# Performance work log

Hardware: AMD Instinct MI355X
Metric: run time of the kernel (lower is better)

Reference implementation:

```python
import jax, jax.numpy as jnp
import numpy as np

H = 100  # hidden size


def _lstm_final_hidden(x, W_ih, W_hh, b_ih, b_hh):
    # x: [B, T, 4] -> final hidden state h_T: [B, H]
    B, T, _ = x.shape
    # Precompute input contribution for all time steps: [B, T, 4H]
    xW = jnp.einsum('btf,gf->btg', x, W_ih) + b_ih + b_hh
    xW = jnp.transpose(xW, (1, 0, 2))  # [T, B, 4H] for scan over time

    def step(carry, xt):
        h, c = carry
        gates = xt + h @ W_hh.T  # [B, 4H]
        i, f, g, o = jnp.split(gates, 4, axis=-1)  # torch gate order: i, f, g, o
        c = jax.nn.sigmoid(f) * c + jax.nn.sigmoid(i) * jnp.tanh(g)
        h = jax.nn.sigmoid(o) * jnp.tanh(c)
        return (h, c), None

    h0 = jnp.zeros((B, H), dtype=x.dtype)
    (hT, _), _ = jax.lax.scan(step, (h0, h0), xW)
    return hT


def setup_inputs() -> dict:
    key = jax.random.key(0)
    k1, k2, k3, k4, k5 = jax.random.split(key, 5)
    n_cells, T = 4096, 128
    short_ttf = jax.random.normal(k1, (n_cells, 3, T, 4), dtype=jnp.float32)
    W_ih = jax.random.normal(k2, (4 * H, 4), dtype=jnp.float32) * 0.1
    # torch init: uniform(-0.05, 0.05) for weight_hh
    W_hh = jax.random.uniform(k3, (4 * H, H), dtype=jnp.float32, minval=-0.05, maxval=0.05)
    b_ih = jax.random.normal(k4, (4 * H,), dtype=jnp.float32) * 0.1
    b_hh = jax.random.normal(k5, (4 * H,), dtype=jnp.float32) * 0.1
    return {"short_ttf": short_ttf, "W_ih": W_ih, "W_hh": W_hh, "b_ih": b_ih, "b_hh": b_hh}


def reference(short_ttf, W_ih, W_hh, b_ih, b_hh):
    # short_ttf: [n_cells, 3, T, 4]. Each of the 3 sub-sequences per cell is run
    # through the same LSTM; last-step hidden states are concatenated -> [n_cells, 3H].
    n_cells, three, T, F = short_ttf.shape
    x = short_ttf.reshape(n_cells * three, T, F)  # batch all sequences together
    hT = _lstm_final_hidden(x, W_ih, W_hh, b_ih, b_hh)  # [n_cells*3, H]
    return hT.reshape(n_cells, three * H)  # [n_cells, 300]
```

## Files before the change

kernel.cpp:

```cpp
#include <hip/hip_runtime.h>
#include <cstdint>


#define H_UNITS 100
#define T_STEPS 128
#define S_BLK   16
#define NSEQ    12288
#define NBLK    (NSEQ / S_BLK)
#define NTILE   25
#define KSTR    136
#define LOG2E   1.4426950408889634f
#define TWO_L   2.8853900817779268f

typedef __attribute__((ext_vector_type(8))) _Float16 halfx8;
typedef __attribute__((ext_vector_type(8))) unsigned short ushortx8;
typedef __attribute__((ext_vector_type(4))) float floatx4;
typedef __attribute__((ext_vector_type(2))) float floatx2;

__device__ __forceinline__ unsigned short f32_to_f16u(float x) {
    _Float16 h = (_Float16)x;
    return __builtin_bit_cast(unsigned short, h);
}
__device__ __forceinline__ float f16u_to_f32(unsigned short u) {
    _Float16 h = __builtin_bit_cast(_Float16, u);
    return (float)h;
}
#if __has_builtin(__builtin_amdgcn_exp2f)
__device__ __forceinline__ float fexp2(float x) { return __builtin_amdgcn_exp2f(x); }
#else
__device__ __forceinline__ float fexp2(float x) { return exp2f(x); }
#endif

__global__ void lstm_prep_pack(const float* __restrict__ W_ih,
                               const float* __restrict__ W_hh,
                               const float* __restrict__ b_ih,
                               const float* __restrict__ b_hh,
                               ushortx8* __restrict__ Bpack) {
    int t = blockIdx.x * 256 + threadIdx.x;
    if (t >= NTILE * 4 * 64) return;
    int lane = t & 63;
    int kc   = (t >> 6) & 3;
    int tile = t >> 8;
    int m    = lane & 15;
    int n;
    if (tile < 24) {
        int pr = tile >> 1, half = tile & 1;
        int reg = m & 3,   qr   = m >> 2;
        int g = (reg >> 1) + 2 * half;
        int u = 8 * pr + 2 * qr + (reg & 1);
        n = g * 100 + u;
    } else {
        n = (m & 3) * 100 + 96 + (m >> 2);
    }
    float sc = (n >= 200 && n < 300) ? (2.0f * LOG2E) : LOG2E;
    int k0 = kc * 32 + ((lane >> 4) & 3) * 8;
    ushortx8 v;
#pragma unroll
    for (int j = 0; j < 8; ++j) {
        int k = k0 + j;
        unsigned short w = 0;
        if (k < 100) {
            w = f32_to_f16u(W_hh[n * 100 + k] * sc);
        } else if (k < 108) {
            w = f32_to_f16u(W_ih[n * 4 + ((k - 100) & 3)] * sc);
        } else if (k < 112) {
            float wf = W_ih[n * 4 + (k - 108)] * sc;
            unsigned short hi = f32_to_f16u(wf);
            w = f32_to_f16u(wf - f16u_to_f32(hi));
        } else if (k == 112) {
            float bb = (b_ih[n] + b_hh[n]) * sc;
            w = f32_to_f16u(bb);
        } else if (k == 113) {
            float bb = (b_ih[n] + b_hh[n]) * sc;
            unsigned short hi = f32_to_f16u(bb);
            w = f32_to_f16u(bb - f16u_to_f32(hi));
        }
        v[j] = w;
    }
    Bpack[t] = v;
}

__global__ void __launch_bounds__(256, 4)
lstm_main(const float* __restrict__ x, const ushortx8* __restrict__ Bpack,
          float* __restrict__ out) {
    __shared__ __align__(16) unsigned short s_A[2][16 * KSTR];
    __shared__ __align__(16) ushortx8       s_W[NTILE * 64];
    __shared__ __align__(16) ushortx8       s_W24[3 * 64];

    const int tid  = threadIdx.x;
    const int lane = tid & 63;
    const int wavu = __builtin_amdgcn_readfirstlane(tid >> 6);
    const int seq0 = blockIdx.x * S_BLK;
    const int m    = lane & 15;
    const int quad = lane >> 4;
    const int q2   = quad << 1;

    halfx8 wfrag[6][3];
#pragma unroll
    for (int s = 0; s < 6; ++s) {
        int tile = 2 * (wavu + (s >> 1) * 4) + (s & 1);
#pragma unroll
        for (int kc = 0; kc < 3; ++kc)
            wfrag[s][kc] = __builtin_bit_cast(halfx8, Bpack[(tile * 4 + kc + 1) * 64 + lane]);
    }
    for (int i = tid; i < NTILE * 64; i += 256)
        s_W[i] = Bpack[(i >> 6) * 256 + (i & 63)];
    if (tid < 3 * 64)
        s_W24[tid] = Bpack[(24 * 4 + 1 + (tid >> 6)) * 64 + (tid & 63)];

    const int rt = tid - 128;
    const int rs = rt & 15, rc = (rt >> 4) & 7;
    const float* xb = x + (size_t)(seq0 + rs) * (T_STEPS * 4) + (rc & 3);

    for (int i = tid; i < (2 * 16 * KSTR) / 2; i += 256)
        ((unsigned int*)s_A)[i] = 0u;
    float x0 = 0.0f;
    if (tid >= 128) x0 = xb[0];
    __syncthreads();
    if (tid >= 128) {
        unsigned short hi = f32_to_f16u(x0);
        if (rc < 4) {
            s_A[0][rs * KSTR + 100 + rc] = hi;
            s_A[0][rs * KSTR + 108 + rc] = hi;
        } else {
            s_A[0][rs * KSTR + 104 + (rc - 4)] =
                f32_to_f16u(x0 - f16u_to_f32(hi));
        }
    } else if (tid < 32) {
        s_A[tid >> 4][(tid & 15) * KSTR + 112] = 0x3C00;
    } else if (tid < 64) {
        int d = tid - 32;
        s_A[d >> 4][(d & 15) * KSTR + 113] = 0x3C00;
    }
    __syncthreads();

    floatx2 cpr[3];
#pragma unroll
    for (int it = 0; it < 3; ++it) cpr[it] = (floatx2){0.0f, 0.0f};
    float c24 = 0.0f;

    const int rowOff = m * KSTR;
    const int aOff   = rowOff + quad * 8;

    for (int t = 0; t < T_STEPS; ++t) {
        const int bR = t & 1;
        const unsigned short* base  = s_A[bR];
        unsigned short*       baseW = s_A[bR ^ 1];

        float xnext = 0.0f;
        if (tid >= 128) {
            int tn = t + 1; if (tn > T_STEPS - 1) tn = T_STEPS - 1;
            xnext = xb[tn * 4];
        }

        halfx8 hh[4];
#pragma unroll
        for (int kc = 0; kc < 4; ++kc)
            hh[kc] = *(const halfx8*)(base + aOff + kc * 32);

        const bool last = (t == T_STEPS - 1);

        auto gemm4 = [&](halfx8 w0, halfx8 w1, halfx8 w2, halfx8 w3) {
            floatx4 a = {0.0f, 0.0f, 0.0f, 0.0f};
            a = __builtin_amdgcn_mfma_f32_16x16x32_f16(w0, hh[0], a, 0, 0, 0);
            a = __builtin_amdgcn_mfma_f32_16x16x32_f16(w1, hh[1], a, 0, 0, 0);
            a = __builtin_amdgcn_mfma_f32_16x16x32_f16(w2, hh[2], a, 0, 0, 0);
            a = __builtin_amdgcn_mfma_f32_16x16x32_f16(w3, hh[3], a, 0, 0, 0);
            return a;
        };

        auto activatePair = [&](floatx4 aA, floatx4 aB, floatx2& cm, int p) {
            floatx2 ei = {fexp2(aA[0]), fexp2(aA[1])};
            floatx2 ef = {fexp2(aA[2]), fexp2(aA[3])};
            floatx2 eg = {fexp2(aB[0]), fexp2(aB[1])};
            floatx2 eo = {fexp2(aB[2]), fexp2(aB[3])};
            floatx2 a  = ei + 1.0f;
            floatx2 b  = ef + 1.0f;
            floatx2 d  = eg + 1.0f;
            floatx2 p1 = eo + 1.0f;
            floatx2 e2s = eg * TWO_L - TWO_L;
            floatx2 q  = a * d;
            floatx2 qb = q * b;
            floatx2 r  = {__builtin_amdgcn_rcpf(qb[0]), __builtin_amdgcn_rcpf(qb[1])};
            floatx2 eib = ei * b;
            floatx2 efq = ef * q;
            floatx2 tt  = eib * e2s;
            floatx2 nm  = efq * cm + tt;
            floatx2 c2  = nm * r;
            cm = c2;
            floatx2 cc = {fminf(c2[0], 115.0f), fminf(c2[1], 115.0f)};
            floatx2 ec = {fexp2(cc[0]), fexp2(cc[1])};
            floatx2 p2 = ec + 1.0f;
            floatx2 nu = ec - 1.0f;
            floatx2 pp = p1 * p2;
            floatx2 r2 = {__builtin_amdgcn_rcpf(pp[0]), __builtin_amdgcn_rcpf(pp[1])};
            floatx2 eon = eo * nu;
            floatx2 hv  = eon * r2;
            if (!last) {
                unsigned int pk = (unsigned int)f32_to_f16u(hv[0]) |
                                  ((unsigned int)f32_to_f16u(hv[1]) << 16);
                *(unsigned int*)&baseW[rowOff + 8 * p + q2] = pk;
            } else {
                *(floatx2*)&out[(size_t)(seq0 + m) * H_UNITS + 8 * p + q2] = hv;
            }
        };

#pragma unroll
        for (int it = 0; it < 3; ++it) {
            int p = wavu + it * 4;
            halfx8 w0A = __builtin_bit_cast(halfx8, s_W[(2 * p) * 64 + lane]);
            halfx8 w0B = __builtin_bit_cast(halfx8, s_W[(2 * p + 1) * 64 + lane]);
            floatx4 aA = gemm4(w0A, wfrag[2 * it][0], wfrag[2 * it][1], wfrag[2 * it][2]);
            floatx4 aB = gemm4(w0B, wfrag[2 * it + 1][0], wfrag[2 * it + 1][1], wfrag[2 * it + 1][2]);
            activatePair(aA, aB, cpr[it], p);
        }

        if (wavu == 0) {
            halfx8 w0 = __builtin_bit_cast(halfx8, s_W[24 * 64 + lane]);
            halfx8 w1 = __builtin_bit_cast(halfx8, s_W24[0 * 64 + lane]);
            halfx8 w2 = __builtin_bit_cast(halfx8, s_W24[1 * 64 + lane]);
            halfx8 w3 = __builtin_bit_cast(halfx8, s_W24[2 * 64 + lane]);
            floatx4 acc = gemm4(w0, w1, w2, w3);
            float ei = fexp2(acc[0]);
            float ef = fexp2(acc[1]);
            float eg = fexp2(acc[2]);
            float eo = fexp2(acc[3]);
            float a  = 1.0f + ei, b = 1.0f + ef;
            float d  = eg + 1.0f;
            float e2s = fmaf(eg, TWO_L, -TWO_L);
            float q  = a * d;
            float r  = __builtin_amdgcn_rcpf(q * b);
            float nm = fmaf(ef * q, c24, (ei * b) * e2s);
            float c2 = nm * r;
            c24 = c2;
            float cc = fminf(c2, 115.0f);
            float ec = fexp2(cc);
            float r2 = __builtin_amdgcn_rcpf((1.0f + eo) * (ec + 1.0f));
            float h  = (eo * (ec - 1.0f)) * r2;
            if (!last) {
                baseW[rowOff + 96 + quad] = f32_to_f16u(h);
            } else {
                out[(size_t)(seq0 + m) * H_UNITS + 96 + quad] = h;
            }
        }

        if (tid >= 128 && !last) {
            unsigned short hi = f32_to_f16u(xnext);
            if (rc < 4) {
                baseW[rs * KSTR + 100 + rc] = hi;
                baseW[rs * KSTR + 108 + rc] = hi;
            } else {
                baseW[rs * KSTR + 104 + (rc - 4)] =
                    f32_to_f16u(xnext - f16u_to_f32(hi));
            }
        }
        __syncthreads();
    }
}

extern "C" void kernel_launch(void* const* d_in, const int* in_sizes, int n_in,
                              void* d_out, int out_size, void* d_ws, size_t ws_size,
                              hipStream_t stream) {
    const float* x    = (const float*)d_in[0];
    const float* W_ih = (const float*)d_in[1];
    const float* W_hh = (const float*)d_in[2];
    const float* b_ih = (const float*)d_in[3];
    const float* b_hh = (const float*)d_in[4];
    ushortx8* Bpack = (ushortx8*)d_ws;

    lstm_prep_pack<<<25, 256, 0, stream>>>(W_ih, W_hh, b_ih, b_hh, Bpack);
    lstm_main<<<NBLK, 256, 0, stream>>>(x, Bpack, (float*)d_out);
}
```

Measured before the change: 289.2 us.

## Split LSTM gate tiles across eight waves per block instead of four

Doubles the block to 512 threads so each of eight waves handles fewer gate tiles per time step. Waves 0-7 keep their first tile pair's weights fully in registers, waves 0-3 take a second pair from shared memory, and wave 4 takes the leftover tile. The aim is a shorter serial critical path per recurrence step through more wave-level parallelism. In exchange it needs more waves per CU and sync across 8 waves, and load is uneven across waves.

```diff
diff --git a/kernel.cpp b/kernel.cpp
--- a/kernel.cpp
+++ b/kernel.cpp
@@ -80,12 +80,11 @@
     Bpack[t] = v;
 }
 
-__global__ void __launch_bounds__(256, 4)
+__global__ void __launch_bounds__(512, 4)
 lstm_main(const float* __restrict__ x, const ushortx8* __restrict__ Bpack,
           float* __restrict__ out) {
     __shared__ __align__(16) unsigned short s_A[2][16 * KSTR];
-    __shared__ __align__(16) ushortx8       s_W[NTILE * 64];
-    __shared__ __align__(16) ushortx8       s_W24[3 * 64];
+    __shared__ __align__(16) ushortx8       s_W[36 * 64];
 
     const int tid  = threadIdx.x;
     const int lane = tid & 63;
@@ -95,29 +94,32 @@
     const int quad = lane >> 4;
     const int q2   = quad << 1;
 
-    halfx8 wfrag[6][3];
+    halfx8 wfA[4], wfB[4];
 #pragma unroll
-    for (int s = 0; s < 6; ++s) {
-        int tile = 2 * (wavu + (s >> 1) * 4) + (s & 1);
-#pragma unroll
-        for (int kc = 0; kc < 3; ++kc)
-            wfrag[s][kc] = __builtin_bit_cast(halfx8, Bpack[(tile * 4 + kc + 1) * 64 + lane]);
-    }
-    for (int i = tid; i < NTILE * 64; i += 256)
-        s_W[i] = Bpack[(i >> 6) * 256 + (i & 63)];
-    if (tid < 3 * 64)
-        s_W24[tid] = Bpack[(24 * 4 + 1 + (tid >> 6)) * 64 + (tid & 63)];
-
-    const int rt = tid - 128;
-    const int rs = rt & 15, rc = (rt >> 4) & 7;
+    for (int kc = 0; kc < 4; ++kc) {
+        wfA[kc] = __builtin_bit_cast(halfx8, Bpack[((2 * wavu) * 4 + kc) * 64 + lane]);
+        wfB[kc] = __builtin_bit_cast(halfx8, Bpack[((2 * wavu + 1) * 4 + kc) * 64 + lane]);
+    }
+
+    for (int i = tid; i < 36 * 64; i += 512) {
+        int f = i >> 6, ln = i & 63;
+        int tile = (f < 32) ? (16 + (f >> 2)) : 24;
+        int kc   = (f < 32) ? (f & 3) : (f - 32);
+        s_W[i] = Bpack[(tile * 4 + kc) * 64 + ln];
+    }
+
+    const int rt   = tid - 320;
+    const bool refr = (rt >= 0) && (rt < 128);
+    const int rtc  = refr ? rt : 0;
+    const int rs   = rtc & 15, rc = (rtc >> 4) & 7;
     const float* xb = x + (size_t)(seq0 + rs) * (T_STEPS * 4) + (rc & 3);
 
-    for (int i = tid; i < (2 * 16 * KSTR) / 2; i += 256)
+    for (int i = tid; i < (2 * 16 * KSTR) / 2; i += 512)
         ((unsigned int*)s_A)[i] = 0u;
     float x0 = 0.0f;
-    if (tid >= 128) x0 = xb[0];
+    if (refr) x0 = xb[0];
     __syncthreads();
-    if (tid >= 128) {
+    if (refr) {
         unsigned short hi = f32_to_f16u(x0);
         if (rc < 4) {
             s_A[0][rs * KSTR + 100 + rc] = hi;
@@ -126,21 +128,19 @@
             s_A[0][rs * KSTR + 104 + (rc - 4)] =
                 f32_to_f16u(x0 - f16u_to_f32(hi));
         }
-    } else if (tid < 32) {
-        s_A[tid >> 4][(tid & 15) * KSTR + 112] = 0x3C00;
     } else if (tid < 64) {
-        int d = tid - 32;
-        s_A[d >> 4][(d & 15) * KSTR + 113] = 0x3C00;
+        int b = tid >> 5, r = (tid >> 1) & 15, col = 112 + (tid & 1);
+        s_A[b][r * KSTR + col] = 0x3C00;
     }
     __syncthreads();
 
-    floatx2 cpr[3];
-#pragma unroll
-    for (int it = 0; it < 3; ++it) cpr[it] = (floatx2){0.0f, 0.0f};
-    float c24 = 0.0f;
+    floatx2 c0 = {0.0f, 0.0f};
+    floatx2 c1 = {0.0f, 0.0f};
+    float   c24 = 0.0f;
 
     const int rowOff = m * KSTR;
     const int aOff   = rowOff + quad * 8;
+    const int hb     = wavu * 512 + lane;
 
     for (int t = 0; t < T_STEPS; ++t) {
         const int bR = t & 1;
@@ -148,7 +148,7 @@
         unsigned short*       baseW = s_A[bR ^ 1];
 
         float xnext = 0.0f;
-        if (tid >= 128) {
+        if (refr) {
             int tn = t + 1; if (tn > T_STEPS - 1) tn = T_STEPS - 1;
             xnext = xb[tn * 4];
         }
@@ -205,21 +205,29 @@
             }
         };
 
-#pragma unroll
-        for (int it = 0; it < 3; ++it) {
-            int p = wavu + it * 4;
-            halfx8 w0A = __builtin_bit_cast(halfx8, s_W[(2 * p) * 64 + lane]);
-            halfx8 w0B = __builtin_bit_cast(halfx8, s_W[(2 * p + 1) * 64 + lane]);
-            floatx4 aA = gemm4(w0A, wfrag[2 * it][0], wfrag[2 * it][1], wfrag[2 * it][2]);
-            floatx4 aB = gemm4(w0B, wfrag[2 * it + 1][0], wfrag[2 * it + 1][1], wfrag[2 * it + 1][2]);
-            activatePair(aA, aB, cpr[it], p);
-        }
-
-        if (wavu == 0) {
-            halfx8 w0 = __builtin_bit_cast(halfx8, s_W[24 * 64 + lane]);
-            halfx8 w1 = __builtin_bit_cast(halfx8, s_W24[0 * 64 + lane]);
-            halfx8 w2 = __builtin_bit_cast(halfx8, s_W24[1 * 64 + lane]);
-            halfx8 w3 = __builtin_bit_cast(halfx8, s_W24[2 * 64 + lane]);
+        {
+            floatx4 aA = gemm4(wfA[0], wfA[1], wfA[2], wfA[3]);
+            floatx4 aB = gemm4(wfB[0], wfB[1], wfB[2], wfB[3]);
+            activatePair(aA, aB, c0, wavu);
+        }
+
+        if (wavu < 4) {
+            halfx8 wa0 = __builtin_bit_cast(halfx8, s_W[hb + 0 * 64]);
+            halfx8 wa1 = __builtin_bit_cast(halfx8, s_W[hb + 1 * 64]);
+            halfx8 wa2 = __builtin_bit_cast(halfx8, s_W[hb + 2 * 64]);
+            halfx8 wa3 = __builtin_bit_cast(halfx8, s_W[hb + 3 * 64]);
+            floatx4 aA = gemm4(wa0, wa1, wa2, wa3);
+            halfx8 wb0 = __builtin_bit_cast(halfx8, s_W[hb + 256 + 0 * 64]);
+            halfx8 wb1 = __builtin_bit_cast(halfx8, s_W[hb + 256 + 1 * 64]);
+            halfx8 wb2 = __builtin_bit_cast(halfx8, s_W[hb + 256 + 2 * 64]);
+            halfx8 wb3 = __builtin_bit_cast(halfx8, s_W[hb + 256 + 3 * 64]);
+            floatx4 aB = gemm4(wb0, wb1, wb2, wb3);
+            activatePair(aA, aB, c1, 8 + wavu);
+        } else if (wavu == 4) {
+            halfx8 w0 = __builtin_bit_cast(halfx8, s_W[2048 + 0 * 64 + lane]);
+            halfx8 w1 = __builtin_bit_cast(halfx8, s_W[2048 + 1 * 64 + lane]);
+            halfx8 w2 = __builtin_bit_cast(halfx8, s_W[2048 + 2 * 64 + lane]);
+            halfx8 w3 = __builtin_bit_cast(halfx8, s_W[2048 + 3 * 64 + lane]);
             floatx4 acc = gemm4(w0, w1, w2, w3);
             float ei = fexp2(acc[0]);
             float ef = fexp2(acc[1]);
@@ -244,7 +252,7 @@
             }
         }
 
-        if (tid >= 128 && !last) {
+        if (refr && !last) {
             unsigned short hi = f32_to_f16u(xnext);
             if (rc < 4) {
                 baseW[rs * KSTR + 100 + rc] = hi;
@@ -269,5 +277,5 @@
     ushortx8* Bpack = (ushortx8*)d_ws;
 
     lstm_prep_pack<<<25, 256, 0, stream>>>(W_ih, W_hh, b_ih, b_hh, Bpack);
-    lstm_main<<<NBLK, 256, 0, stream>>>(x, Bpack, (float*)d_out);
-}
+    lstm_main<<<NBLK, 512, 0, stream>>>(x, Bpack, (float*)d_out);
+}
```

Measured after the change: 283.2 us (median of 2 runs). 2.1% less time.

## Run each 16-sequence LSTM block on a single wavefront with register-resident weights

Applied to the files above, without the earlier changes.

Replaces the 4-wave block with a single 64-thread wavefront that computes all 25 gate tiles for its 16 sequences. 20 tiles of W_hh are held in registers and the rest are read from shared memory. Using one wave removes the per-step __syncthreads and the double-buffered hidden-state array, so h is updated in place. The cost is much higher register pressure, possible spills, and fewer waves to hide MFMA and transcendental latency, since each wave now does four times the serial work per step.

```diff
diff --git a/kernel.cpp b/kernel.cpp
--- a/kernel.cpp
+++ b/kernel.cpp
@@ -80,83 +80,68 @@
     Bpack[t] = v;
 }
 
-__global__ void __launch_bounds__(256, 4)
+__global__ void __launch_bounds__(64, 1)
 lstm_main(const float* __restrict__ x, const ushortx8* __restrict__ Bpack,
           float* __restrict__ out) {
-    __shared__ __align__(16) unsigned short s_A[2][16 * KSTR];
-    __shared__ __align__(16) ushortx8       s_W[NTILE * 64];
-    __shared__ __align__(16) ushortx8       s_W24[3 * 64];
-
-    const int tid  = threadIdx.x;
-    const int lane = tid & 63;
-    const int wavu = __builtin_amdgcn_readfirstlane(tid >> 6);
-    const int seq0 = blockIdx.x * S_BLK;
+    __shared__ __align__(16) unsigned short s_h[16 * KSTR];
+    __shared__ __align__(16) ushortx8       s_W[20 * 64];
+
+    const int lane = threadIdx.x & 63;
     const int m    = lane & 15;
     const int quad = lane >> 4;
     const int q2   = quad << 1;
-
-    halfx8 wfrag[6][3];
-#pragma unroll
-    for (int s = 0; s < 6; ++s) {
-        int tile = 2 * (wavu + (s >> 1) * 4) + (s & 1);
-#pragma unroll
-        for (int kc = 0; kc < 3; ++kc)
-            wfrag[s][kc] = __builtin_bit_cast(halfx8, Bpack[(tile * 4 + kc + 1) * 64 + lane]);
-    }
-    for (int i = tid; i < NTILE * 64; i += 256)
-        s_W[i] = Bpack[(i >> 6) * 256 + (i & 63)];
-    if (tid < 3 * 64)
-        s_W24[tid] = Bpack[(24 * 4 + 1 + (tid >> 6)) * 64 + (tid & 63)];
-
-    const int rt = tid - 128;
-    const int rs = rt & 15, rc = (rt >> 4) & 7;
-    const float* xb = x + (size_t)(seq0 + rs) * (T_STEPS * 4) + (rc & 3);
-
-    for (int i = tid; i < (2 * 16 * KSTR) / 2; i += 256)
-        ((unsigned int*)s_A)[i] = 0u;
-    float x0 = 0.0f;
-    if (tid >= 128) x0 = xb[0];
-    __syncthreads();
-    if (tid >= 128) {
+    const int seq0 = blockIdx.x * S_BLK;
+
+    halfx8 wfA[10][4], wfB[10][4];
+#pragma unroll
+    for (int p = 0; p < 10; ++p)
+#pragma unroll
+        for (int kc = 0; kc < 4; ++kc) {
+            wfA[p][kc] = __builtin_bit_cast(halfx8, Bpack[((2 * p) * 4 + kc) * 64 + lane]);
+            wfB[p][kc] = __builtin_bit_cast(halfx8, Bpack[((2 * p + 1) * 4 + kc) * 64 + lane]);
+        }
+    for (int i = lane; i < 20 * 64; i += 64) {
+        int f = i >> 6, ln = i & 63;
+        int tile = (f < 16) ? (20 + (f >> 2)) : 24;
+        int kc   = (f < 16) ? (f & 3) : (f - 16);
+        s_W[i] = Bpack[(tile * 4 + kc) * 64 + ln];
+    }
+
+    for (int i = lane; i < (16 * KSTR) / 2; i += 64)
+        ((unsigned int*)s_h)[i] = 0u;
+
+    const float* xb = x + (size_t)(seq0 + m) * (T_STEPS * 4) + quad;
+    {
+        float x0 = xb[0];
         unsigned short hi = f32_to_f16u(x0);
-        if (rc < 4) {
-            s_A[0][rs * KSTR + 100 + rc] = hi;
-            s_A[0][rs * KSTR + 108 + rc] = hi;
-        } else {
-            s_A[0][rs * KSTR + 104 + (rc - 4)] =
-                f32_to_f16u(x0 - f16u_to_f32(hi));
-        }
-    } else if (tid < 32) {
-        s_A[tid >> 4][(tid & 15) * KSTR + 112] = 0x3C00;
-    } else if (tid < 64) {
-        int d = tid - 32;
-        s_A[d >> 4][(d & 15) * KSTR + 113] = 0x3C00;
-    }
-    __syncthreads();
-
-    floatx2 cpr[3];
-#pragma unroll
-    for (int it = 0; it < 3; ++it) cpr[it] = (floatx2){0.0f, 0.0f};
+        __syncthreads();
+        s_h[m * KSTR + 100 + quad] = hi;
+        s_h[m * KSTR + 108 + quad] = hi;
+        s_h[m * KSTR + 104 + quad] = f32_to_f16u(x0 - f16u_to_f32(hi));
+        if (lane < 32)
+            s_h[(lane >> 1) * KSTR + 112 + (lane & 1)] = 0x3C00;
+    }
+
+    floatx2 cpr[12];
+#pragma unroll
+    for (int p = 0; p < 12; ++p) cpr[p] = (floatx2){0.0f, 0.0f};
     float c24 = 0.0f;
 
     const int rowOff = m * KSTR;
     const int aOff   = rowOff + quad * 8;
 
     for (int t = 0; t < T_STEPS; ++t) {
-        const int bR = t & 1;
-        const unsigned short* base  = s_A[bR];
-        unsigned short*       baseW = s_A[bR ^ 1];
-
-        float xnext = 0.0f;
-        if (tid >= 128) {
-            int tn = t + 1; if (tn > T_STEPS - 1) tn = T_STEPS - 1;
-            xnext = xb[tn * 4];
-        }
+        int tn = t + 1; if (tn > T_STEPS - 1) tn = T_STEPS - 1;
+        float xn = xb[tn * 4];
+
+        __threadfence_block();
 
         halfx8 hh[4];
 #pragma unroll
         for (int kc = 0; kc < 4; ++kc)
-            hh[kc] = *(const halfx8*)(base + aOff + kc * 32);
+            hh[kc] = *(const halfx8*)(s_h + aOff + kc * 32);
+
+        asm volatile("" ::: "memory");
 
         const bool last = (t == T_STEPS - 1);
 
@@ -199,27 +184,38 @@
             if (!last) {
                 unsigned int pk = (unsigned int)f32_to_f16u(hv[0]) |
                                   ((unsigned int)f32_to_f16u(hv[1]) << 16);
-                *(unsigned int*)&baseW[rowOff + 8 * p + q2] = pk;
+                *(unsigned int*)&s_h[rowOff + 8 * p + q2] = pk;
             } else {
                 *(floatx2*)&out[(size_t)(seq0 + m) * H_UNITS + 8 * p + q2] = hv;
             }
         };
 
 #pragma unroll
-        for (int it = 0; it < 3; ++it) {
-            int p = wavu + it * 4;
-            halfx8 w0A = __builtin_bit_cast(halfx8, s_W[(2 * p) * 64 + lane]);
-            halfx8 w0B = __builtin_bit_cast(halfx8, s_W[(2 * p + 1) * 64 + lane]);
-            floatx4 aA = gemm4(w0A, wfrag[2 * it][0], wfrag[2 * it][1], wfrag[2 * it][2]);
-            floatx4 aB = gemm4(w0B, wfrag[2 * it + 1][0], wfrag[2 * it + 1][1], wfrag[2 * it + 1][2]);
-            activatePair(aA, aB, cpr[it], p);
-        }
-
-        if (wavu == 0) {
-            halfx8 w0 = __builtin_bit_cast(halfx8, s_W[24 * 64 + lane]);
-            halfx8 w1 = __builtin_bit_cast(halfx8, s_W24[0 * 64 + lane]);
-            halfx8 w2 = __builtin_bit_cast(halfx8, s_W24[1 * 64 + lane]);
-            halfx8 w3 = __builtin_bit_cast(halfx8, s_W24[2 * 64 + lane]);
+        for (int p = 0; p < 10; ++p) {
+            floatx4 aA = gemm4(wfA[p][0], wfA[p][1], wfA[p][2], wfA[p][3]);
+            floatx4 aB = gemm4(wfB[p][0], wfB[p][1], wfB[p][2], wfB[p][3]);
+            activatePair(aA, aB, cpr[p], p);
+        }
+#pragma unroll
+        for (int p = 10; p < 12; ++p) {
+            int fb = (p - 10) * 8;
+            halfx8 wa0 = __builtin_bit_cast(halfx8, s_W[(fb + 0) * 64 + lane]);
+            halfx8 wa1 = __builtin_bit_cast(halfx8, s_W[(fb + 1) * 64 + lane]);
+            halfx8 wa2 = __builtin_bit_cast(halfx8, s_W[(fb + 2) * 64 + lane]);
+            halfx8 wa3 = __builtin_bit_cast(halfx8, s_W[(fb + 3) * 64 + lane]);
+            floatx4 aA = gemm4(wa0, wa1, wa2, wa3);
+            halfx8 wb0 = __builtin_bit_cast(halfx8, s_W[(fb + 4) * 64 + lane]);
+            halfx8 wb1 = __builtin_bit_cast(halfx8, s_W[(fb + 5) * 64 + lane]);
+            halfx8 wb2 = __builtin_bit_cast(halfx8, s_W[(fb + 6) * 64 + lane]);
+            halfx8 wb3 = __builtin_bit_cast(halfx8, s_W[(fb + 7) * 64 + lane]);
+            floatx4 aB = gemm4(wb0, wb1, wb2, wb3);
+            activatePair(aA, aB, cpr[p], p);
+        }
+        {
+            halfx8 w0 = __builtin_bit_cast(halfx8, s_W[(16 + 0) * 64 + lane]);
+            halfx8 w1 = __builtin_bit_cast(halfx8, s_W[(16 + 1) * 64 + lane]);
+            halfx8 w2 = __builtin_bit_cast(halfx8, s_W[(16 + 2) * 64 + lane]);
+            halfx8 w3 = __builtin_bit_cast(halfx8, s_W[(16 + 3) * 64 + lane]);
             floatx4 acc = gemm4(w0, w1, w2, w3);
             float ei = fexp2(acc[0]);
             float ef = fexp2(acc[1]);
@@ -238,23 +234,18 @@
             float r2 = __builtin_amdgcn_rcpf((1.0f + eo) * (ec + 1.0f));
             float h  = (eo * (ec - 1.0f)) * r2;
             if (!last) {
-                baseW[rowOff + 96 + quad] = f32_to_f16u(h);
+                s_h[rowOff + 96 + quad] = f32_to_f16u(h);
             } else {
                 out[(size_t)(seq0 + m) * H_UNITS + 96 + quad] = h;
             }
         }
 
-        if (tid >= 128 && !last) {
-            unsigned short hi = f32_to_f16u(xnext);
-            if (rc < 4) {
-                baseW[rs * KSTR + 100 + rc] = hi;
-                baseW[rs * KSTR + 108 + rc] = hi;
-            } else {
-                baseW[rs * KSTR + 104 + (rc - 4)] =
-                    f32_to_f16u(xnext - f16u_to_f32(hi));
-            }
-        }
-        __syncthreads();
+        if (!last) {
+            unsigned short hi = f32_to_f16u(xn);
+            s_h[rowOff + 100 + quad] = hi;
+            s_h[rowOff + 108 + quad] = hi;
+            s_h[rowOff + 104 + quad] = f32_to_f16u(xn - f16u_to_f32(hi));
+        }
     }
 }
 
@@ -269,5 +260,5 @@
     ushortx8* Bpack = (ushortx8*)d_ws;
 
     lstm_prep_pack<<<25, 256, 0, stream>>>(W_ih, W_hh, b_ih, b_hh, Bpack);
-    lstm_main<<<NBLK, 256, 0, stream>>>(x, Bpack, (float*)d_out);
-}
+    lstm_main<<<NBLK, 64, 0, stream>>>(x, Bpack, (float*)d_out);
+}
```

Result: slower. 383.0 us (+32.4%).
